# Kernel optimization log

Hardware: AMD Instinct MI355X
Metric: run time of the kernel (lower is better)

Reference implementation:

```python
import jax, jax.numpy as jnp
import numpy as np

NUM_NODES = 50000
NUM_RELS = 47        # 2*23 + 1 after enrich()
EMB_DIM = 1600
WEIGHTS_SIZE = 16
NUM_CLASSES = 50
BASES = 40
NUM_EDGES = 1600000


def setup_inputs() -> dict:
    key = jax.random.key(0)
    ks = jax.random.split(key, 8)
    return {
        "node_embeddings": jax.random.normal(ks[0], (NUM_NODES, EMB_DIM), jnp.float32),
        "comps1": jax.random.normal(ks[1], (NUM_RELS, BASES), jnp.float32),
        "bases1": jax.random.normal(ks[2], (BASES, EMB_DIM, WEIGHTS_SIZE), jnp.float32) * 0.05,
        "comps2": jax.random.normal(ks[3], (NUM_RELS, BASES), jnp.float32),
        "bases2": jax.random.normal(ks[4], (BASES, WEIGHTS_SIZE, NUM_CLASSES), jnp.float32) * 0.05,
        "bias1": jnp.zeros((WEIGHTS_SIZE,), jnp.float32),
        "bias2": jnp.zeros((NUM_CLASSES,), jnp.float32),
        "rows": jax.random.randint(ks[5], (NUM_EDGES,), 0, NUM_NODES, jnp.int32),
        "cols": jax.random.randint(ks[6], (NUM_EDGES,), 0, NUM_RELS * NUM_NODES, jnp.int32),
    }


def _spmm(rows, cols, vals, h_rel):
    # hor_graph @ h_rel : h_rel is (R*N, d); out[n] = sum_e vals[e] * h_rel[cols[e]]
    msgs = vals[:, None] * h_rel[cols]              # (E, d)
    return jax.ops.segment_sum(msgs, rows, num_segments=NUM_NODES)


def reference(node_embeddings, comps1, bases1, comps2, bases2, bias1, bias2, rows, cols):
    R, N = NUM_RELS, NUM_NODES
    # normalization: 1 / row-sums of vertical adjacency == 1 / counts per hor column
    cnt = jax.ops.segment_sum(jnp.ones_like(cols, jnp.float32), cols, num_segments=R * N)
    vals = 1.0 / cnt[cols]                          # (E,)

    # layer 1: basis-decomposed per-relation transform
    w1 = jnp.einsum('rb,bio->rio', comps1, bases1)  # (R, emb, ws)
    h = jnp.einsum('ni,rio->rno', node_embeddings, w1)  # (R, N, ws)
    h = h.reshape(R * N, WEIGHTS_SIZE)
    h = _spmm(rows, cols, vals, h)                  # (N, ws)
    h = jax.nn.relu(h + bias1)

    # layer 2
    w2 = jnp.einsum('rb,bio->rio', comps2, bases2)  # (R, ws, C)
    h = jnp.einsum('ni,rio->rno', h, w2)            # (R, N, C)
    h = h.reshape(R * N, NUM_CLASSES)
    h = _spmm(rows, cols, vals, h)                  # (N, C)
    return h + bias2
```

## Files before the change

kernel.cpp:

```cpp
#include <hip/hip_runtime.h>
#include <hip/hip_bf16.h>

#define NN 50000
#define RR 47
#define ED 1600
#define WS 16
#define NC 50
#define NB 40
#define NE 1600000
#define WJ (RR*WS)
#define WJP 768

#define GEMM_NBLK 2346
#define SCAN_B 1024
#define SCAN_NBLK ((NN + SCAN_B - 1) / SCAN_B)
#define L2ROWS 16

typedef unsigned short ushort_t;
typedef short s16x8 __attribute__((ext_vector_type(8)));
typedef float f32x4 __attribute__((ext_vector_type(4)));

__device__ __forceinline__ ushort_t f2bf(float f) {
    __hip_bfloat16 h = __float2bfloat16(f);
    ushort_t u;
    __builtin_memcpy(&u, &h, 2);
    return u;
}
__device__ __forceinline__ float bf2f(ushort_t u) {
    unsigned v = ((unsigned)u) << 16;
    float f;
    __builtin_memcpy(&f, &v, 4);
    return f;
}

__device__ __forceinline__ void async_copy16(const ushort_t* g, ushort_t* l) {
    __builtin_amdgcn_global_load_lds(
        (const __attribute__((address_space(1))) unsigned int*)g,
        (__attribute__((address_space(3))) unsigned int*)l,
        16, 0, 0);
}

__global__ void cast_kernel(const float* __restrict__ X, ushort_t* __restrict__ A) {
    int idx = blockIdx.x * blockDim.x + threadIdx.x;
    if (idx >= (NN * ED) / 4) return;
    float4 v = ((const float4*)X)[idx];
    ushort_t* p = &A[idx * 4];
    p[0] = f2bf(v.x); p[1] = f2bf(v.y); p[2] = f2bf(v.z); p[3] = f2bf(v.w);
}

__global__ void count_kernel(const int* __restrict__ cols, float* __restrict__ cnt) {
    int e = blockIdx.x * blockDim.x + threadIdx.x;
    if (e < NE) atomicAdd(&cnt[cols[e]], 1.0f);
}

__global__ void wbigbt_kernel(const float* __restrict__ comps1, const float* __restrict__ bases1,
                              ushort_t* __restrict__ WbigB) {
    int idx = blockIdx.x * blockDim.x + threadIdx.x;
    if (idx >= WJP * ED) return;
    int j = idx / ED;
    int i = idx - j * ED;
    float s = 0.f;
    if (j < WJ) {
        int r = j >> 4;
        int o = j & 15;
#pragma unroll
        for (int b = 0; b < NB; ++b)
            s += comps1[r * NB + b] * bases1[(b * ED + i) * WS + o];
    }
    WbigB[idx] = f2bf(s);
}

__global__ __launch_bounds__(256) void mfma_gemm_kernel(const ushort_t* __restrict__ A,
                                                        const ushort_t* __restrict__ B,
                                                        ushort_t* __restrict__ C) {
    __shared__ ushort_t Abuf[128 * 32];
    __shared__ ushort_t Bbuf[128 * 32];

    const int bid = blockIdx.x;
    const int q = GEMM_NBLK / 8, rm = GEMM_NBLK % 8;
    const int xcd = bid & 7, loc = bid >> 3;
    const int sbid = (xcd < rm ? xcd * (q + 1) : rm * (q + 1) + (xcd - rm) * q) + loc;
    const int mb = sbid / 6;
    const int nb = sbid - mb * 6;

    const int t = threadIdx.x;
    const int lane = t & 63;
    const int wave = t >> 6;
    const int m0 = mb * 128;
    const int n0 = nb * 128;
    const int wm = (wave & 1) * 64;
    const int wn = (wave >> 1) * 64;

    const int arow0 = t >> 2,        akp0 = (t & 3) * 8;
    const int arow1 = (t + 256) >> 2, akp1 = ((t + 256) & 3) * 8;
    int gm0 = m0 + arow0; if (gm0 >= NN) gm0 = NN - 1;
    int gm1 = m0 + arow1; if (gm1 >= NN) gm1 = NN - 1;
    const ushort_t* ap0 = &A[(size_t)gm0 * ED + akp0];
    const ushort_t* ap1 = &A[(size_t)gm1 * ED + akp1];
    const ushort_t* bp0 = &B[(size_t)(n0 + arow0) * ED + akp0];
    const ushort_t* bp1 = &B[(size_t)(n0 + arow1) * ED + akp1];

    f32x4 acc[4][4];
#pragma unroll
    for (int i = 0; i < 4; ++i)
#pragma unroll
        for (int j = 0; j < 4; ++j) acc[i][j] = (f32x4){0.f, 0.f, 0.f, 0.f};

    const int frow = lane & 15;
    const int fk = (lane >> 4) * 8;

    for (int k0 = 0; k0 < ED; k0 += 32) {
        async_copy16(ap0 + k0, &Abuf[t * 8]);
        async_copy16(ap1 + k0, &Abuf[(t + 256) * 8]);
        async_copy16(bp0 + k0, &Bbuf[t * 8]);
        async_copy16(bp1 + k0, &Bbuf[(t + 256) * 8]);
        __syncthreads();

        s16x8 af[4], bf[4];
#pragma unroll
        for (int mt = 0; mt < 4; ++mt)
            af[mt] = *(const s16x8*)&Abuf[(wm + mt * 16 + frow) * 32 + fk];
#pragma unroll
        for (int nt = 0; nt < 4; ++nt)
            bf[nt] = *(const s16x8*)&Bbuf[(wn + nt * 16 + frow) * 32 + fk];
#pragma unroll
        for (int mt = 0; mt < 4; ++mt)
#pragma unroll
            for (int nt = 0; nt < 4; ++nt)
                acc[mt][nt] = __builtin_amdgcn_mfma_f32_16x16x32_bf16(af[mt], bf[nt], acc[mt][nt], 0, 0, 0);
        __syncthreads();
    }

    const int cm = (lane >> 4) * 4;
    const int cn = lane & 15;
#pragma unroll
    for (int mt = 0; mt < 4; ++mt) {
#pragma unroll
        for (int i = 0; i < 4; ++i) {
            int gm = m0 + wm + mt * 16 + cm + i;
            if (gm >= NN) continue;
#pragma unroll
            for (int nt = 0; nt < 4; ++nt) {
                int gn = n0 + wn + nt * 16 + cn;
                if (gn < WJ) C[(size_t)gm * WJ + gn] = f2bf(acc[mt][nt][i]);
            }
        }
    }
}

__global__ void hist_kernel(const int* __restrict__ rows, int* __restrict__ rcnt) {
    int e = blockIdx.x * blockDim.x + threadIdx.x;
    if (e < NE) atomicAdd(&rcnt[rows[e]], 1);
}

__global__ __launch_bounds__(SCAN_B) void scan1_kernel(const int* __restrict__ rcnt,
                                                       int* __restrict__ ptr,
                                                       int* __restrict__ bsum) {
    __shared__ int buf[2][SCAN_B];
    int t = threadIdx.x, base = blockIdx.x * SCAN_B;
    int v = (base + t < NN) ? rcnt[base + t] : 0;
    buf[0][t] = v;
    __syncthreads();
    int src = 0;
    for (int off = 1; off < SCAN_B; off <<= 1) {
        int x = buf[src][t];
        if (t >= off) x += buf[src][t - off];
        buf[src ^ 1][t] = x;
        src ^= 1;
        __syncthreads();
    }
    int incl = buf[src][t];
    if (base + t < NN) ptr[base + t] = incl - v;
    if (t == SCAN_B - 1) bsum[blockIdx.x] = incl;
}

__global__ void scan2_kernel(int* __restrict__ bsum, int* __restrict__ ptr) {
    if (threadIdx.x == 0 && blockIdx.x == 0) {
        int run = 0;
        for (int i = 0; i < SCAN_NBLK; ++i) { int v = bsum[i]; bsum[i] = run; run += v; }
        ptr[NN] = run;
    }
}

__global__ void scan3_kernel(const int* __restrict__ bsum, int* __restrict__ ptr) {
    int idx = blockIdx.x * blockDim.x + threadIdx.x;
    if (idx < NN) ptr[idx] += bsum[idx >> 10];
}

__global__ void scatter_kernel(const int* __restrict__ rows, const int* __restrict__ cols,
                               const float* __restrict__ cnt, const int* __restrict__ ptr,
                               int* __restrict__ fill, int* __restrict__ ecol,
                               float* __restrict__ eval) {
    int e = blockIdx.x * blockDim.x + threadIdx.x;
    if (e >= NE) return;
    int rw = rows[e];
    int pos = ptr[rw] + atomicAdd(&fill[rw], 1);
    int c = cols[e];
    ecol[pos] = c;
    eval[pos] = 1.0f / cnt[c];
}

__global__ __launch_bounds__(256) void spmm1_csr_kernel(const int* __restrict__ ptr,
        const int* __restrict__ ecol, const float* __restrict__ eval,
        const ushort_t* __restrict__ hrel, const float* __restrict__ bias1,
        float* __restrict__ h1) {
    int t = threadIdx.x;
    int wave = t >> 6, lane = t & 63;
    int m = blockIdx.x * 4 + wave;
    int start = ptr[m], end = ptr[m + 1];
    int o = lane & 15, sub = lane >> 4;
    float acc = 0.f;
    for (int e0 = start; e0 < end; e0 += 4) {
        int e = e0 + sub;
        if (e < end) {
            int col = ecol[e];
            float v = eval[e];
            int r = col / NN;
            int n = col - r * NN;
            acc += v * bf2f(hrel[(size_t)n * WJ + r * WS + o]);
        }
    }
    acc += __shfl_xor(acc, 16);
    acc += __shfl_xor(acc, 32);
    if (lane < 16) {
        float hv = acc + bias1[o];
        h1[m * WS + o] = hv > 0.f ? hv : 0.f;
    }
}

__global__ void w2p_kernel(const float* __restrict__ comps2, const float* __restrict__ bases2,
                           float* __restrict__ w2p) {
    int idx = blockIdx.x * blockDim.x + threadIdx.x;
    if (idx >= WJ * 64) return;
    int k = idx >> 6;
    int c = idx & 63;
    float s = 0.f;
    if (c < NC) {
        int r = k >> 4;
        int o = k & 15;
#pragma unroll
        for (int b = 0; b < NB; ++b)
            s += comps2[r * NB + b] * bases2[(b * WS + o) * NC + c];
    }
    w2p[idx] = s;
}

__global__ __launch_bounds__(256) void layer2_kernel(const int* __restrict__ ptr,
        const int* __restrict__ ecol, const float* __restrict__ eval,
        const float* __restrict__ h1, const float* __restrict__ w2p,
        const float* __restrict__ bias2, float* __restrict__ out) {
    __shared__ float gt[L2ROWS][WJ];
    __shared__ float Bs[16][68];

    int t = threadIdx.x;
    int m0 = blockIdx.x * L2ROWS;

    for (int i = t; i < L2ROWS * WJ; i += 256) ((float*)gt)[i] = 0.f;
    __syncthreads();

    int wave = t >> 6, lane = t & 63;
    int o = lane & 15, sub = lane >> 4;
    for (int lr = wave * 4; lr < wave * 4 + 4; ++lr) {
        int m = m0 + lr;
        if (m >= NN) break;
        int start = ptr[m], end = ptr[m + 1];
        for (int e0 = start; e0 < end; e0 += 4) {
            int e = e0 + sub;
            if (e < end) {
                int col = ecol[e];
                float v = eval[e];
                int r = col / NN;
                int n = col - r * NN;
                atomicAdd(&gt[lr][r * WS + o], v * h1[n * WS + o]);
            }
        }
    }
    __syncthreads();

    int i = t >> 4, tx = t & 15;
    float acc[4] = {0.f, 0.f, 0.f, 0.f};
    for (int k0 = 0; k0 < WJ; k0 += 16) {
        *(float4*)&Bs[t >> 4][(t & 15) * 4] =
            *(const float4*)&w2p[(k0 + (t >> 4)) * 64 + (t & 15) * 4];
        __syncthreads();
#pragma unroll
        for (int k = 0; k < 16; ++k) {
            float a = gt[i][k0 + k];
            float4 b = *(const float4*)&Bs[k][tx * 4];
            acc[0] += a * b.x; acc[1] += a * b.y; acc[2] += a * b.z; acc[3] += a * b.w;
        }
        __syncthreads();
    }
    int m = m0 + i;
    if (m < NN) {
#pragma unroll
        for (int j = 0; j < 4; ++j) {
            int c = tx * 4 + j;
            if (c < NC) out[m * NC + c] = acc[j] + bias2[c];
        }
    }
}

extern "C" void kernel_launch(void* const* d_in, const int* in_sizes, int n_in,
                              void* d_out, int out_size, void* d_ws, size_t ws_size,
                              hipStream_t stream) {
    const float* X      = (const float*)d_in[0];
    const float* comps1 = (const float*)d_in[1];
    const float* bases1 = (const float*)d_in[2];
    const float* comps2 = (const float*)d_in[3];
    const float* bases2 = (const float*)d_in[4];
    const float* bias1  = (const float*)d_in[5];
    const float* bias2  = (const float*)d_in[6];
    const int*   rows   = (const int*)d_in[7];
    const int*   cols   = (const int*)d_in[8];
    float* out = (float*)d_out;

    char* ws = (char*)d_ws;
    float*    cnt    = (float*)   (ws + 0);
    ushort_t* Abf    = (ushort_t*)(ws + 9400064);
    int*      rowptr = (int*)     (ws + 9400064);
    int*      rcnt   = (int*)     (ws + 9600128);
    int*      fill   = (int*)     (ws + 9800192);
    int*      bsum   = (int*)     (ws + 10000256);
    int*      ecol   = (int*)     (ws + 10000512);
    float*    eval   = (float*)   (ws + 16400512);
    ushort_t* WbigB  = (ushort_t*)(ws + 169400064);
    ushort_t* hrel   = (ushort_t*)(ws + 171857664);
    float*    h1     = (float*)   (ws + 247057664);
    float*    w2p    = (float*)   (ws + 250257664);

    hipMemsetAsync(cnt, 0, (size_t)RR * NN * 4, stream);

    cast_kernel<<<(NN * ED / 4 + 255) / 256, 256, 0, stream>>>(X, Abf);
    count_kernel<<<(NE + 255) / 256, 256, 0, stream>>>(cols, cnt);
    wbigbt_kernel<<<(WJP * ED + 255) / 256, 256, 0, stream>>>(comps1, bases1, WbigB);

    mfma_gemm_kernel<<<GEMM_NBLK, 256, 0, stream>>>(Abf, WbigB, hrel);

    hipMemsetAsync(rcnt, 0, (size_t)NN * 4, stream);
    hipMemsetAsync(fill, 0, (size_t)NN * 4, stream);
    hist_kernel<<<(NE + 255) / 256, 256, 0, stream>>>(rows, rcnt);
    scan1_kernel<<<SCAN_NBLK, SCAN_B, 0, stream>>>(rcnt, rowptr, bsum);
    scan2_kernel<<<1, 64, 0, stream>>>(bsum, rowptr);
    scan3_kernel<<<(NN + 255) / 256, 256, 0, stream>>>(bsum, rowptr);
    scatter_kernel<<<(NE + 255) / 256, 256, 0, stream>>>(rows, cols, cnt, rowptr, fill, ecol, eval);

    spmm1_csr_kernel<<<NN / 4, 256, 0, stream>>>(rowptr, ecol, eval, hrel, bias1, h1);

    w2p_kernel<<<(WJ * 64 + 255) / 256, 256, 0, stream>>>(comps2, bases2, w2p);
    layer2_kernel<<<(NN + L2ROWS - 1) / L2ROWS, 256, 0, stream>>>(rowptr, ecol, eval, h1, w2p, bias2, out);
}
```

Measured before the change: 1.321 ms.

## Use bf16 MFMA for layer-2 dense product and vectorize sparse gathers

Layer 2's dense product (16 rows by 768 by 50) now runs on the bf16 MFMA 16x16x32 instruction. It reads a transposed bf16 copy of W2, replacing the fp32 LDS-tiled loop. The edge scatter into shared memory iterates over the block's whole contiguous edge range using a new per-edge row index array, which balances work across threads instead of per-row loops. Layer-1 SpMM loads four bf16 values per lane and handles 16 edges per wave iteration. This trades fp32 accuracy in layer 2 for bf16 and adds an extra edge array write.

```diff
diff --git a/kernel.cpp b/kernel.cpp
--- a/kernel.cpp
+++ b/kernel.cpp
@@ -15,9 +15,11 @@
 #define SCAN_B 1024
 #define SCAN_NBLK ((NN + SCAN_B - 1) / SCAN_B)
 #define L2ROWS 16
+#define GTS 772
 
 typedef unsigned short ushort_t;
 typedef short s16x8 __attribute__((ext_vector_type(8)));
+typedef short s16x4 __attribute__((ext_vector_type(4)));
 typedef float f32x4 __attribute__((ext_vector_type(4)));
 
 __device__ __forceinline__ ushort_t f2bf(float f) {
@@ -190,7 +192,7 @@
 __global__ void scatter_kernel(const int* __restrict__ rows, const int* __restrict__ cols,
                                const float* __restrict__ cnt, const int* __restrict__ ptr,
                                int* __restrict__ fill, int* __restrict__ ecol,
-                               float* __restrict__ eval) {
+                               float* __restrict__ eval, ushort_t* __restrict__ erow) {
     int e = blockIdx.x * blockDim.x + threadIdx.x;
     if (e >= NE) return;
     int rw = rows[e];
@@ -198,6 +200,7 @@
     int c = cols[e];
     ecol[pos] = c;
     eval[pos] = 1.0f / cnt[c];
+    erow[pos] = (ushort_t)rw;
 }
 
 __global__ __launch_bounds__(256) void spmm1_csr_kernel(const int* __restrict__ ptr,
@@ -208,95 +211,109 @@
     int wave = t >> 6, lane = t & 63;
     int m = blockIdx.x * 4 + wave;
     int start = ptr[m], end = ptr[m + 1];
-    int o = lane & 15, sub = lane >> 4;
-    float acc = 0.f;
-    for (int e0 = start; e0 < end; e0 += 4) {
+    int sub = lane >> 2;
+    int oq = (lane & 3) * 4;
+    float acc[4] = {0.f, 0.f, 0.f, 0.f};
+    for (int e0 = start; e0 < end; e0 += 16) {
         int e = e0 + sub;
         if (e < end) {
             int col = ecol[e];
             float v = eval[e];
             int r = col / NN;
             int n = col - r * NN;
-            acc += v * bf2f(hrel[(size_t)n * WJ + r * WS + o]);
-        }
-    }
-    acc += __shfl_xor(acc, 16);
-    acc += __shfl_xor(acc, 32);
-    if (lane < 16) {
-        float hv = acc + bias1[o];
-        h1[m * WS + o] = hv > 0.f ? hv : 0.f;
-    }
-}
-
-__global__ void w2p_kernel(const float* __restrict__ comps2, const float* __restrict__ bases2,
-                           float* __restrict__ w2p) {
+            s16x4 hv = *(const s16x4*)&hrel[(size_t)n * WJ + r * WS + oq];
+#pragma unroll
+            for (int j = 0; j < 4; ++j)
+                acc[j] += v * bf2f((ushort_t)hv[j]);
+        }
+    }
+#pragma unroll
+    for (int d = 4; d <= 32; d <<= 1)
+#pragma unroll
+        for (int j = 0; j < 4; ++j)
+            acc[j] += __shfl_xor(acc[j], d);
+    if (lane < 4) {
+        float4 hv;
+        float* hp = (float*)&hv;
+#pragma unroll
+        for (int j = 0; j < 4; ++j) {
+            float x = acc[j] + bias1[oq + j];
+            hp[j] = x > 0.f ? x : 0.f;
+        }
+        *(float4*)&h1[m * WS + oq] = hv;
+    }
+}
+
+__global__ void w2pt_kernel(const float* __restrict__ comps2, const float* __restrict__ bases2,
+                            ushort_t* __restrict__ w2pT) {
     int idx = blockIdx.x * blockDim.x + threadIdx.x;
-    if (idx >= WJ * 64) return;
-    int k = idx >> 6;
-    int c = idx & 63;
+    if (idx >= 64 * 768) return;
+    int c = idx / 768;
+    int k = idx - c * 768;
     float s = 0.f;
-    if (c < NC) {
+    if (c < NC && k < WJ) {
         int r = k >> 4;
         int o = k & 15;
 #pragma unroll
         for (int b = 0; b < NB; ++b)
             s += comps2[r * NB + b] * bases2[(b * WS + o) * NC + c];
     }
-    w2p[idx] = s;
+    w2pT[idx] = f2bf(s);
 }
 
 __global__ __launch_bounds__(256) void layer2_kernel(const int* __restrict__ ptr,
         const int* __restrict__ ecol, const float* __restrict__ eval,
-        const float* __restrict__ h1, const float* __restrict__ w2p,
+        const ushort_t* __restrict__ erow,
+        const float* __restrict__ h1, const ushort_t* __restrict__ w2pT,
         const float* __restrict__ bias2, float* __restrict__ out) {
-    __shared__ float gt[L2ROWS][WJ];
-    __shared__ float Bs[16][68];
+    __shared__ float gt[L2ROWS][GTS];
 
     int t = threadIdx.x;
     int m0 = blockIdx.x * L2ROWS;
 
-    for (int i = t; i < L2ROWS * WJ; i += 256) ((float*)gt)[i] = 0.f;
+    for (int i = t; i < L2ROWS * GTS; i += 256) ((float*)gt)[i] = 0.f;
     __syncthreads();
 
+    {
+        int estart = ptr[m0];
+        int eend = ptr[m0 + L2ROWS];
+        int g = t >> 4, o = t & 15;
+        for (int e = estart + g; e < eend; e += 16) {
+            int col = ecol[e];
+            float v = eval[e];
+            int lr = (int)erow[e] - m0;
+            int r = col / NN;
+            int n = col - r * NN;
+            atomicAdd(&gt[lr][r * WS + o], v * h1[n * WS + o]);
+        }
+    }
+    __syncthreads();
+
     int wave = t >> 6, lane = t & 63;
-    int o = lane & 15, sub = lane >> 4;
-    for (int lr = wave * 4; lr < wave * 4 + 4; ++lr) {
-        int m = m0 + lr;
-        if (m >= NN) break;
-        int start = ptr[m], end = ptr[m + 1];
-        for (int e0 = start; e0 < end; e0 += 4) {
-            int e = e0 + sub;
-            if (e < end) {
-                int col = ecol[e];
-                float v = eval[e];
-                int r = col / NN;
-                int n = col - r * NN;
-                atomicAdd(&gt[lr][r * WS + o], v * h1[n * WS + o]);
-            }
-        }
-    }
-    __syncthreads();
-
-    int i = t >> 4, tx = t & 15;
-    float acc[4] = {0.f, 0.f, 0.f, 0.f};
-    for (int k0 = 0; k0 < WJ; k0 += 16) {
-        *(float4*)&Bs[t >> 4][(t & 15) * 4] =
-            *(const float4*)&w2p[(k0 + (t >> 4)) * 64 + (t & 15) * 4];
-        __syncthreads();
-#pragma unroll
-        for (int k = 0; k < 16; ++k) {
-            float a = gt[i][k0 + k];
-            float4 b = *(const float4*)&Bs[k][tx * 4];
-            acc[0] += a * b.x; acc[1] += a * b.y; acc[2] += a * b.z; acc[3] += a * b.w;
-        }
-        __syncthreads();
-    }
-    int m = m0 + i;
-    if (m < NN) {
-#pragma unroll
-        for (int j = 0; j < 4; ++j) {
-            int c = tx * 4 + j;
-            if (c < NC) out[m * NC + c] = acc[j] + bias2[c];
+    int arow = lane & 15;
+    int kx = (lane >> 4) * 8;
+    int n0 = wave * 16;
+    f32x4 acc = (f32x4){0.f, 0.f, 0.f, 0.f};
+    const ushort_t* bbase = &w2pT[(size_t)(n0 + arow) * 768 + kx];
+    for (int k0 = 0; k0 < 768; k0 += 32) {
+        f32x4 a0 = *(const f32x4*)&gt[arow][k0 + kx];
+        f32x4 a1 = *(const f32x4*)&gt[arow][k0 + kx + 4];
+        s16x8 af;
+        af[0] = (short)f2bf(a0[0]); af[1] = (short)f2bf(a0[1]);
+        af[2] = (short)f2bf(a0[2]); af[3] = (short)f2bf(a0[3]);
+        af[4] = (short)f2bf(a1[0]); af[5] = (short)f2bf(a1[1]);
+        af[6] = (short)f2bf(a1[2]); af[7] = (short)f2bf(a1[3]);
+        s16x8 bf = *(const s16x8*)&bbase[k0];
+        acc = __builtin_amdgcn_mfma_f32_16x16x32_bf16(af, bf, acc, 0, 0, 0);
+    }
+    int cn = n0 + (lane & 15);
+    if (cn < NC) {
+        int rbase = (lane >> 4) * 4;
+        float b2 = bias2[cn];
+#pragma unroll
+        for (int i = 0; i < 4; ++i) {
+            int m = m0 + rbase + i;
+            out[m * NC + cn] = acc[i] + b2;
         }
     }
 }
@@ -324,10 +341,11 @@
     int*      bsum   = (int*)     (ws + 10000256);
     int*      ecol   = (int*)     (ws + 10000512);
     float*    eval   = (float*)   (ws + 16400512);
+    ushort_t* erow   = (ushort_t*)(ws + 22800512);
     ushort_t* WbigB  = (ushort_t*)(ws + 169400064);
     ushort_t* hrel   = (ushort_t*)(ws + 171857664);
     float*    h1     = (float*)   (ws + 247057664);
-    float*    w2p    = (float*)   (ws + 250257664);
+    ushort_t* w2pT   = (ushort_t*)(ws + 250257664);
 
     hipMemsetAsync(cnt, 0, (size_t)RR * NN * 4, stream);
 
@@ -343,10 +361,10 @@
     scan1_kernel<<<SCAN_NBLK, SCAN_B, 0, stream>>>(rcnt, rowptr, bsum);
     scan2_kernel<<<1, 64, 0, stream>>>(bsum, rowptr);
     scan3_kernel<<<(NN + 255) / 256, 256, 0, stream>>>(bsum, rowptr);
-    scatter_kernel<<<(NE + 255) / 256, 256, 0, stream>>>(rows, cols, cnt, rowptr, fill, ecol, eval);
+    scatter_kernel<<<(NE + 255) / 256, 256, 0, stream>>>(rows, cols, cnt, rowptr, fill, ecol, eval, erow);
 
     spmm1_csr_kernel<<<NN / 4, 256, 0, stream>>>(rowptr, ecol, eval, hrel, bias1, h1);
 
-    w2p_kernel<<<(WJ * 64 + 255) / 256, 256, 0, stream>>>(comps2, bases2, w2p);
-    layer2_kernel<<<(NN + L2ROWS - 1) / L2ROWS, 256, 0, stream>>>(rowptr, ecol, eval, h1, w2p, bias2, out);
-}
+    w2pt_kernel<<<(64 * 768 + 255) / 256, 256, 0, stream>>>(comps2, bases2, w2pT);
+    layer2_kernel<<<NN / L2ROWS, 256, 0, stream>>>(rowptr, ecol, eval, erow, h1, w2pT, bias2, out);
+}
```

Measured after the change: 1.189 ms. -10.0%, faster.
